# Performance work log

Measured on AMD Instinct MI355X. Metric: run time of the kernel, lower is better.

The kernel has to match this reference:

```python
import jax, jax.numpy as jnp
import numpy as np

B, D, K = 4096, 2048, 8
RANGE_MIN, RANGE_MAX = -5.0, 5.0
MIN_BIN, MIN_SLOPE, MAX_SLOPE = 1e-3, 1e-3, 10.0


def setup_inputs() -> dict:
    key = jax.random.key(0)
    kx, kp = jax.random.split(key)
    x = jax.random.normal(kx, (B, D), dtype=jnp.float32)
    params = jax.random.normal(kp, (D, 3 * K + 1), dtype=jnp.float32) * 0.01
    return {"x": x, "params": params}


def _normalize_params(params):
    # params: [D, 3K+1] -> x_knots [D,K+1], y_knots [D,K+1], slopes [D,K+1]
    widths_raw = params[:, :K]
    heights_raw = params[:, K:2 * K]
    slopes_raw = params[:, 2 * K:]
    total_range = RANGE_MAX - RANGE_MIN
    remaining = total_range - K * MIN_BIN
    ws = jax.nn.sigmoid(widths_raw)
    widths = MIN_BIN + ws * remaining / jnp.sum(ws, axis=-1, keepdims=True)
    hs = jax.nn.sigmoid(heights_raw)
    heights = MIN_BIN + hs * remaining / jnp.sum(hs, axis=-1, keepdims=True)
    slopes = MIN_SLOPE + jax.nn.sigmoid(slopes_raw) * (MAX_SLOPE - MIN_SLOPE)
    pad = jnp.full((params.shape[0], 1), RANGE_MIN, dtype=params.dtype)
    x_knots = jnp.concatenate([pad, RANGE_MIN + jnp.cumsum(widths, axis=-1)], axis=-1)
    y_knots = jnp.concatenate([pad, RANGE_MIN + jnp.cumsum(heights, axis=-1)], axis=-1)
    return x_knots, y_knots, slopes


def reference(x, params):
    # x: [B, D]; params: [D, 3K+1] -> (y [B,D], total_logdet [B])
    x_knots, y_knots, slopes = _normalize_params(params)
    d_idx = jnp.arange(params.shape[0])[None, :]  # [1, D]

    below = x <= RANGE_MIN
    above = x >= RANGE_MAX
    s0 = slopes[:, 0][None, :]   # [1, D]
    sK = slopes[:, -1][None, :]  # [1, D]
    y_below = RANGE_MIN + (x - RANGE_MIN) * s0
    y_above = RANGE_MAX + (x - RANGE_MAX) * sK

    # searchsorted(x_knots[1:-1], x, side='right') == count of interior knots <= x
    bin_idx = jnp.sum(x_knots[None, :, 1:-1] <= x[:, :, None], axis=-1)  # [B, D]
    bin_idx = jnp.clip(bin_idx, 0, K - 1)

    x_k = x_knots[d_idx, bin_idx]
    x_k1 = x_knots[d_idx, bin_idx + 1]
    y_k = y_knots[d_idx, bin_idx]
    y_k1 = y_knots[d_idx, bin_idx + 1]
    d_k = slopes[d_idx, bin_idx]
    d_k1 = slopes[d_idx, bin_idx + 1]

    width = x_k1 - x_k
    height = y_k1 - y_k
    xi = (x - x_k) / width
    s = height / width
    xi1 = 1.0 - xi
    numerator = s * xi * xi + d_k * xi * xi1
    denominator = s + (d_k1 + d_k - 2.0 * s) * xi * xi1
    y_spline = y_k + height * numerator / denominator
    deriv_num = s * s * (d_k1 * xi * xi + 2.0 * s * xi * xi1 + d_k * xi1 * xi1)
    derivative = deriv_num / (denominator * denominator)

    y = jnp.where(below, y_below, jnp.where(above, y_above, y_spline))
    logdet = jnp.where(below, jnp.log(s0),
                       jnp.where(above, jnp.log(sK), jnp.log(derivative)))
    return y, jnp.sum(logdet, axis=-1)
```

## Files before the change

kernel.cpp:

```cpp
#include <hip/hip_runtime.h>
#include <hip/hip_bf16.h>

#define KBINS 8
#define DDIM 2048
#define BROWS 4096
#define NPAR (3 * KBINS + 1)
#define ROWS_PER_BLOCK 16

__device__ __forceinline__ float fast_rcp(float a) {
    float r = __builtin_amdgcn_rcpf(a);
    r = r * (2.0f - a * r);
    return r;
}

__global__ __launch_bounds__(256) void normalize_params_kernel(
        const float* __restrict__ params, float* __restrict__ tab) {
    const int d = blockIdx.x * blockDim.x + threadIdx.x;
    if (d >= DDIM) return;
    const float* p = params + d * NPAR;

    const float RMIN = -5.0f, RMAX = 5.0f;
    const float MIN_BIN = 1e-3f, MIN_SLOPE = 1e-3f, MAX_SLOPE = 10.0f;
    const float remaining = (RMAX - RMIN) - KBINS * MIN_BIN;

    float wsig[KBINS], hsig[KBINS];
    float wsum = 0.0f, hsum = 0.0f;
#pragma unroll
    for (int k = 0; k < KBINS; ++k) {
        wsig[k] = 1.0f / (1.0f + expf(-p[k]));
        wsum += wsig[k];
    }
#pragma unroll
    for (int k = 0; k < KBINS; ++k) {
        hsig[k] = 1.0f / (1.0f + expf(-p[KBINS + k]));
        hsum += hsig[k];
    }
    const float wscale = remaining / wsum;
    const float hscale = remaining / hsum;

    float* xk_t = tab;
    float* yk_t = tab + (KBINS + 1) * DDIM;
    float* sl_t = tab + 2 * (KBINS + 1) * DDIM;

    xk_t[d] = RMIN;
    yk_t[d] = RMIN;
    float cx = RMIN, cy = RMIN;
#pragma unroll
    for (int k = 0; k < KBINS; ++k) {
        cx += MIN_BIN + wsig[k] * wscale;
        cy += MIN_BIN + hsig[k] * hscale;
        xk_t[(k + 1) * DDIM + d] = cx;
        yk_t[(k + 1) * DDIM + d] = cy;
    }
#pragma unroll
    for (int k = 0; k <= KBINS; ++k) {
        float sr = p[2 * KBINS + k];
        sl_t[k * DDIM + d] = MIN_SLOPE + (MAX_SLOPE - MIN_SLOPE) / (1.0f + expf(-sr));
    }
}

__global__ __launch_bounds__(256) void rqs_kernel(
        const float* __restrict__ x_in, const float* __restrict__ tab,
        float* __restrict__ y_out, float* __restrict__ logdet) {
    const int d = (blockIdx.x & 7) * 256 + (int)threadIdx.x;
    const int b0 = (int)(blockIdx.x >> 3) * ROWS_PER_BLOCK;

    const float RMIN = -5.0f, RMAX = 5.0f;

    const float* xk_t = tab;
    const float* yk_t = tab + (KBINS + 1) * DDIM;
    const float* sl_t = tab + 2 * (KBINS + 1) * DDIM;

    float xk[KBINS + 1], yk[KBINS + 1], sl[KBINS + 1];
#pragma unroll
    for (int k = 0; k <= KBINS; ++k) {
        xk[k] = xk_t[k * DDIM + d];
        yk[k] = yk_t[k * DDIM + d];
        sl[k] = sl_t[k * DDIM + d];
    }
    float wd[KBINS], hd[KBINS];
#pragma unroll
    for (int k = 0; k < KBINS; ++k) {
        wd[k] = xk[k + 1] - xk[k];
        hd[k] = yk[k + 1] - yk[k];
    }
    const float log_s0 = __logf(sl[0]);
    const float log_sK = __logf(sl[KBINS]);

    for (int r = 0; r < ROWS_PER_BLOCK; ++r) {
        const int b = b0 + r;
        const int idx = b * DDIM + d;
        const float x = x_in[idx];

        float x_k = xk[0], w = wd[0], y_k = yk[0], h = hd[0];
        float dk = sl[0], dk1 = sl[1];
#pragma unroll
        for (int j = 1; j < KBINS; ++j) {
            const bool c = xk[j] <= x;
            x_k = c ? xk[j] : x_k;
            w   = c ? wd[j] : w;
            y_k = c ? yk[j] : y_k;
            h   = c ? hd[j] : h;
            dk  = c ? sl[j] : dk;
            dk1 = c ? sl[j + 1] : dk1;
        }

        const float inv_w = fast_rcp(w);
        const float xi  = (x - x_k) * inv_w;
        const float s   = h * inv_w;
        const float xi1 = 1.0f - xi;
        const float xx  = xi * xi1;

        const float num = s * xi * xi + dk * xx;
        const float den = s + (dk1 + dk - 2.0f * s) * xx;
        const float inv_den = fast_rcp(den);

        float y  = fmaf(h * num, inv_den, y_k);
        const float inner = dk1 * xi * xi + 2.0f * s * xx + dk * xi1 * xi1;
        float ld = 2.0f * __logf(s) + __logf(inner) - 2.0f * __logf(den);

        if (x <= RMIN) { y = fmaf(x - RMIN, sl[0], RMIN); ld = log_s0; }
        else if (x >= RMAX) { y = fmaf(x - RMAX, sl[KBINS], RMAX); ld = log_sK; }

        y_out[idx] = y;

        float v = ld;
#pragma unroll
        for (int off = 32; off > 0; off >>= 1) v += __shfl_down(v, off);
        if ((threadIdx.x & 63) == 0) atomicAdd(&logdet[b], v);
    }
}

extern "C" void kernel_launch(void* const* d_in, const int* in_sizes, int n_in,
                              void* d_out, int out_size, void* d_ws, size_t ws_size,
                              hipStream_t stream) {
    const float* x = (const float*)d_in[0];
    const float* params = (const float*)d_in[1];
    float* out = (float*)d_out;
    float* y_out = out;
    float* logdet = out + (size_t)BROWS * DDIM;
    float* tab = (float*)d_ws;

    hipMemsetAsync(logdet, 0, BROWS * sizeof(float), stream);

    normalize_params_kernel<<<DDIM / 256, 256, 0, stream>>>(params, tab);

    const int grid = 8 * (BROWS / ROWS_PER_BLOCK);
    rqs_kernel<<<grid, 256, 0, stream>>>(x, tab, y_out, logdet);
}
```

Measured before the change: 113.6 us.

## Fuse param normalization into RQS kernel with LDS knot table and block reduction

```diff
diff --git a/kernel.cpp b/kernel.cpp
--- a/kernel.cpp
+++ b/kernel.cpp
@@ -13,98 +13,83 @@
     return r;
 }
 
-__global__ __launch_bounds__(256) void normalize_params_kernel(
-        const float* __restrict__ params, float* __restrict__ tab) {
-    const int d = blockIdx.x * blockDim.x + threadIdx.x;
-    if (d >= DDIM) return;
-    const float* p = params + d * NPAR;
+__device__ __forceinline__ float fsigmoid(float t) {
+    return fast_rcp(1.0f + __expf(-t));
+}
+
+__global__ __launch_bounds__(256) void rqs_kernel(
+        const float* __restrict__ x_in, const float* __restrict__ params,
+        float* __restrict__ y_out, float* __restrict__ logdet) {
+    const int tid = (int)threadIdx.x;
+    const int d = (blockIdx.x & 7) * 256 + tid;
+    const int b0 = (int)(blockIdx.x >> 3) * ROWS_PER_BLOCK;
 
     const float RMIN = -5.0f, RMAX = 5.0f;
     const float MIN_BIN = 1e-3f, MIN_SLOPE = 1e-3f, MAX_SLOPE = 10.0f;
     const float remaining = (RMAX - RMIN) - KBINS * MIN_BIN;
 
-    float wsig[KBINS], hsig[KBINS];
+    __shared__ float lt[27][256];
+    __shared__ float red[ROWS_PER_BLOCK][4];
+
+    const float* p = params + d * NPAR;
+    float pr[NPAR];
+#pragma unroll
+    for (int i = 0; i < NPAR; ++i) pr[i] = p[i];
+
+    float ws[KBINS], hs[KBINS], sl[KBINS + 1];
     float wsum = 0.0f, hsum = 0.0f;
 #pragma unroll
-    for (int k = 0; k < KBINS; ++k) {
-        wsig[k] = 1.0f / (1.0f + expf(-p[k]));
-        wsum += wsig[k];
-    }
+    for (int k = 0; k < KBINS; ++k) { ws[k] = fsigmoid(pr[k]); wsum += ws[k]; }
 #pragma unroll
-    for (int k = 0; k < KBINS; ++k) {
-        hsig[k] = 1.0f / (1.0f + expf(-p[KBINS + k]));
-        hsum += hsig[k];
-    }
-    const float wscale = remaining / wsum;
-    const float hscale = remaining / hsum;
+    for (int k = 0; k < KBINS; ++k) { hs[k] = fsigmoid(pr[KBINS + k]); hsum += hs[k]; }
+#pragma unroll
+    for (int k = 0; k <= KBINS; ++k)
+        sl[k] = MIN_SLOPE + (MAX_SLOPE - MIN_SLOPE) * fsigmoid(pr[2 * KBINS + k]);
 
-    float* xk_t = tab;
-    float* yk_t = tab + (KBINS + 1) * DDIM;
-    float* sl_t = tab + 2 * (KBINS + 1) * DDIM;
+    const float wscale = remaining * fast_rcp(wsum);
+    const float hscale = remaining * fast_rcp(hsum);
 
-    xk_t[d] = RMIN;
-    yk_t[d] = RMIN;
+    lt[0][tid] = RMIN;
+    lt[9][tid] = RMIN;
+    float xkr[KBINS];
     float cx = RMIN, cy = RMIN;
 #pragma unroll
     for (int k = 0; k < KBINS; ++k) {
-        cx += MIN_BIN + wsig[k] * wscale;
-        cy += MIN_BIN + hsig[k] * hscale;
-        xk_t[(k + 1) * DDIM + d] = cx;
-        yk_t[(k + 1) * DDIM + d] = cy;
+        cx += MIN_BIN + ws[k] * wscale;
+        cy += MIN_BIN + hs[k] * hscale;
+        lt[1 + k][tid] = cx;
+        lt[10 + k][tid] = cy;
+        if (k < KBINS - 1) xkr[k + 1] = cx;
     }
 #pragma unroll
-    for (int k = 0; k <= KBINS; ++k) {
-        float sr = p[2 * KBINS + k];
-        sl_t[k * DDIM + d] = MIN_SLOPE + (MAX_SLOPE - MIN_SLOPE) / (1.0f + expf(-sr));
-    }
-}
+    for (int k = 0; k <= KBINS; ++k) lt[18 + k][tid] = sl[k];
 
-__global__ __launch_bounds__(256) void rqs_kernel(
-        const float* __restrict__ x_in, const float* __restrict__ tab,
-        float* __restrict__ y_out, float* __restrict__ logdet) {
-    const int d = (blockIdx.x & 7) * 256 + (int)threadIdx.x;
-    const int b0 = (int)(blockIdx.x >> 3) * ROWS_PER_BLOCK;
+    const float s0 = sl[0], sK = sl[KBINS];
+    const float log_s0 = __logf(s0), log_sK = __logf(sK);
+    __syncthreads();
 
-    const float RMIN = -5.0f, RMAX = 5.0f;
+    float xv[ROWS_PER_BLOCK];
+#pragma unroll
+    for (int r = 0; r < ROWS_PER_BLOCK; ++r)
+        xv[r] = x_in[(size_t)(b0 + r) * DDIM + d];
 
-    const float* xk_t = tab;
-    const float* yk_t = tab + (KBINS + 1) * DDIM;
-    const float* sl_t = tab + 2 * (KBINS + 1) * DDIM;
+    float ldv[ROWS_PER_BLOCK];
+#pragma unroll
+    for (int r = 0; r < ROWS_PER_BLOCK; ++r) {
+        const float x = xv[r];
+        int bin = 0;
+#pragma unroll
+        for (int j = 1; j < KBINS; ++j) bin += (xkr[j] <= x) ? 1 : 0;
 
-    float xk[KBINS + 1], yk[KBINS + 1], sl[KBINS + 1];
-#pragma unroll
-    for (int k = 0; k <= KBINS; ++k) {
-        xk[k] = xk_t[k * DDIM + d];
-        yk[k] = yk_t[k * DDIM + d];
-        sl[k] = sl_t[k * DDIM + d];
-    }
-    float wd[KBINS], hd[KBINS];
-#pragma unroll
-    for (int k = 0; k < KBINS; ++k) {
-        wd[k] = xk[k + 1] - xk[k];
-        hd[k] = yk[k + 1] - yk[k];
-    }
-    const float log_s0 = __logf(sl[0]);
-    const float log_sK = __logf(sl[KBINS]);
+        const float x_k  = lt[bin][tid];
+        const float x_k1 = lt[bin + 1][tid];
+        const float y_k  = lt[9 + bin][tid];
+        const float y_k1 = lt[10 + bin][tid];
+        const float dk   = lt[18 + bin][tid];
+        const float dk1  = lt[19 + bin][tid];
 
-    for (int r = 0; r < ROWS_PER_BLOCK; ++r) {
-        const int b = b0 + r;
-        const int idx = b * DDIM + d;
-        const float x = x_in[idx];
-
-        float x_k = xk[0], w = wd[0], y_k = yk[0], h = hd[0];
-        float dk = sl[0], dk1 = sl[1];
-#pragma unroll
-        for (int j = 1; j < KBINS; ++j) {
-            const bool c = xk[j] <= x;
-            x_k = c ? xk[j] : x_k;
-            w   = c ? wd[j] : w;
-            y_k = c ? yk[j] : y_k;
-            h   = c ? hd[j] : h;
-            dk  = c ? sl[j] : dk;
-            dk1 = c ? sl[j + 1] : dk1;
-        }
-
+        const float w = x_k1 - x_k;
+        const float h = y_k1 - y_k;
         const float inv_w = fast_rcp(w);
         const float xi  = (x - x_k) * inv_w;
         const float s   = h * inv_w;
@@ -115,19 +100,38 @@
         const float den = s + (dk1 + dk - 2.0f * s) * xx;
         const float inv_den = fast_rcp(den);
 
-        float y  = fmaf(h * num, inv_den, y_k);
+        const float y_sp = fmaf(h * num, inv_den, y_k);
         const float inner = dk1 * xi * xi + 2.0f * s * xx + dk * xi1 * xi1;
-        float ld = 2.0f * __logf(s) + __logf(inner) - 2.0f * __logf(den);
+        const float t = s * inv_den;
+        const float der = t * t * inner;
 
-        if (x <= RMIN) { y = fmaf(x - RMIN, sl[0], RMIN); ld = log_s0; }
-        else if (x >= RMAX) { y = fmaf(x - RMAX, sl[KBINS], RMAX); ld = log_sK; }
+        const bool below = x <= RMIN;
+        const bool above = x >= RMAX;
+        float y  = below ? fmaf(x - RMIN, s0, RMIN)
+                 : above ? fmaf(x - RMAX, sK, RMAX) : y_sp;
+        float ld = below ? log_s0 : above ? log_sK : __logf(der);
 
-        y_out[idx] = y;
+        y_out[(size_t)(b0 + r) * DDIM + d] = y;
+        ldv[r] = ld;
+    }
 
-        float v = ld;
 #pragma unroll
-        for (int off = 32; off > 0; off >>= 1) v += __shfl_down(v, off);
-        if ((threadIdx.x & 63) == 0) atomicAdd(&logdet[b], v);
+    for (int off = 32; off > 0; off >>= 1) {
+#pragma unroll
+        for (int r = 0; r < ROWS_PER_BLOCK; ++r)
+            ldv[r] += __shfl_down(ldv[r], off);
+    }
+    const int wid = tid >> 6, lane = tid & 63;
+    if (lane == 0) {
+#pragma unroll
+        for (int r = 0; r < ROWS_PER_BLOCK; ++r) red[r][wid] = ldv[r];
+    }
+    __syncthreads();
+    if (wid == 0) {
+        float v = red[lane >> 2][lane & 3];
+        v += __shfl_down(v, 1);
+        v += __shfl_down(v, 2);
+        if ((lane & 3) == 0) atomicAdd(&logdet[b0 + (lane >> 2)], v);
     }
 }
 
@@ -139,12 +143,9 @@
     float* out = (float*)d_out;
     float* y_out = out;
     float* logdet = out + (size_t)BROWS * DDIM;
-    float* tab = (float*)d_ws;
 
     hipMemsetAsync(logdet, 0, BROWS * sizeof(float), stream);
 
-    normalize_params_kernel<<<DDIM / 256, 256, 0, stream>>>(params, tab);
-
     const int grid = 8 * (BROWS / ROWS_PER_BLOCK);
-    rqs_kernel<<<grid, 256, 0, stream>>>(x, tab, y_out, logdet);
+    rqs_kernel<<<grid, 256, 0, stream>>>(x, params, y_out, logdet);
 }
```

Result: faster. 100.8 us (-11.3%).
